# Performance work log

Measured on AMD Instinct MI355X. Metric: run time of the kernel, lower is better.

Reference implementation:

```python
import jax, jax.numpy as jnp
import numpy as np

N_NODES = 50000
N_EDGES = 800000
C_IN = 128
C_OUT = 64
C_HID = 2 * C_OUT  # 128


def setup_inputs() -> dict:
    key = jax.random.key(0)
    ks = jax.random.split(key, 8)
    x = jax.random.normal(ks[0], (N_NODES, C_IN), dtype=jnp.float32)
    edge_index = jax.random.randint(ks[1], (2, N_EDGES), 0, N_NODES, dtype=jnp.int64)
    s1 = 1.0 / np.sqrt(C_IN)
    s2 = 1.0 / np.sqrt(C_HID)
    s3 = 1.0 / np.sqrt(C_OUT)
    W1 = jax.random.uniform(ks[2], (C_IN, C_HID), jnp.float32, -s1, s1)
    b1 = jnp.zeros((C_HID,), jnp.float32)
    W2 = jax.random.uniform(ks[3], (C_HID, C_OUT), jnp.float32, -s2, s2)
    b2 = jnp.zeros((C_OUT,), jnp.float32)
    Wb = jax.random.uniform(ks[4], (1, C_OUT, C_OUT), jnp.float32, -s3, s3)
    bb = jax.random.uniform(ks[5], (1,), jnp.float32, -s3, s3)
    return {"x": x, "edge_index": edge_index, "W1": W1, "b1": b1,
            "W2": W2, "b2": b2, "Wb": Wb, "bb": bb}


def gcn_conv(x, W, b, src, dst, n_nodes):
    # PyG GCNConv: h = x @ W; add self-loops; symmetric normalization D^-1/2 (A+I) D^-1/2.
    h = x @ W  # [N, F]
    ones = jnp.ones((src.shape[0],), h.dtype)
    deg = jax.ops.segment_sum(ones, dst, num_segments=n_nodes) + 1.0  # +1 for self-loop
    dinv = jax.lax.rsqrt(deg)
    norm = dinv[src] * dinv[dst]  # [E]
    msgs = h[src] * norm[:, None]  # [E, F]
    agg = jax.ops.segment_sum(msgs, dst, num_segments=n_nodes)
    # self-loop contribution: norm_ii = 1/deg_i
    agg = agg + h * (1.0 / deg)[:, None]
    return agg + b


def reference(x, edge_index, W1, b1, W2, b2, Wb, bb):
    src = edge_index[0]
    dst = edge_index[1]
    n = x.shape[0]
    # encode
    h = jax.nn.relu(gcn_conv(x, W1, b1, src, dst, n))
    z = gcn_conv(h, W2, b2, src, dst, n)  # [N, C_OUT]
    # decode: bilinear on (z[src], z[dst]) -> sigmoid
    zs = z[src]  # [E, C_OUT]
    zd = z[dst]  # [E, C_OUT]
    logits = jnp.einsum('ec,ocd,ed->eo', zs, Wb, zd) + bb  # [E, 1]
    return jax.nn.sigmoid(logits)
```

## Files before the change

### kernel.cpp

```cpp
#include <hip/hip_runtime.h>
#include <hip/hip_bf16.h>


#define N_NODES 50000
#define BSH 7
#define BSZ 128
#define NBUCK ((N_NODES + BSZ - 1) / BSZ)
#define EPB 4096
#define CAP 3072
#define DSPLIT 4

typedef unsigned int u32;
typedef unsigned short u16;
typedef unsigned long long u64;

typedef __attribute__((ext_vector_type(8))) short bf16x8;
typedef __attribute__((ext_vector_type(4))) float f32x4;
union frag_u { bf16x8 f; u32 u[4]; uint4 v; };

__device__ __forceinline__ float bflo(u32 u) { return __uint_as_float(u << 16); }
__device__ __forceinline__ float bfhi(u32 u) { return __uint_as_float(u & 0xffff0000u); }
__device__ __forceinline__ u32 f2bf(float f) {
    u32 b = __float_as_uint(f);
    return (b + 0x7fffu + ((b >> 16) & 1u)) >> 16;
}
__device__ __forceinline__ u32 pack2(float a, float b) { return f2bf(a) | (f2bf(b) << 16); }

__global__ __launch_bounds__(256) void gemm1_scatter(
        const float* __restrict__ X, const float* __restrict__ W,
        u16* __restrict__ O, int n_rows, int gblk,
        const int* __restrict__ src, const int* __restrict__ dst,
        int* __restrict__ bcur, u64* __restrict__ pair, int E) {
    constexpr int K = 128, NOUT = 128;
    constexpr int KP = K + 8;
    constexpr int NT = NOUT / 16;
    constexpr int KS = K / 32;
    __shared__ __align__(16) char smem[NOUT * KP * 2 * sizeof(u16)];
    int t = threadIdx.x;

    if ((int)blockIdx.x < gblk) {
        u16* Wt_hi = (u16*)smem;
        u16* Wt_lo = Wt_hi + NOUT * KP;
        for (int i4 = t; i4 < K * NOUT / 4; i4 += 256) {
            int k = (i4 * 4) / NOUT;
            int n0 = (i4 * 4) % NOUT;
            float4 w4 = *(const float4*)&W[(size_t)k * NOUT + n0];
            float wv[4] = {w4.x, w4.y, w4.z, w4.w};
#pragma unroll
            for (int q = 0; q < 4; q++) {
                u32 hi = f2bf(wv[q]);
                u32 lo = f2bf(wv[q] - bflo(hi));
                Wt_hi[(n0 + q) * KP + k] = (u16)hi;
                Wt_lo[(n0 + q) * KP + k] = (u16)lo;
            }
        }
        __syncthreads();

        int wave = t >> 6;
        int lane = t & 63;
        int m16 = lane & 15;
        int quad = lane >> 4;
        int row0 = blockIdx.x * 128 + wave * 32;

        f32x4 acc[2][NT] = {};
        for (int ks = 0; ks < KS; ks++) {
            frag_u a_hi[2], a_lo[2];
#pragma unroll
            for (int mt = 0; mt < 2; mt++) {
                int row = row0 + mt * 16 + m16;
                row = row < n_rows ? row : n_rows - 1;
                const float* Xp = X + (size_t)row * K + ks * 32 + quad * 8;
                float4 x0 = *(const float4*)Xp;
                float4 x1 = *(const float4*)(Xp + 4);
                float xv[8] = {x0.x, x0.y, x0.z, x0.w, x1.x, x1.y, x1.z, x1.w};
#pragma unroll
                for (int p = 0; p < 4; p++) {
                    u32 h0 = f2bf(xv[2 * p]), h1 = f2bf(xv[2 * p + 1]);
                    a_hi[mt].u[p] = h0 | (h1 << 16);
                    a_lo[mt].u[p] = pack2(xv[2 * p] - bflo(h0), xv[2 * p + 1] - bflo(h1));
                }
            }
#pragma unroll
            for (int nt = 0; nt < NT; nt++) {
                int n = nt * 16 + m16;
                frag_u b_hi, b_lo;
                b_hi.v = *(const uint4*)&Wt_hi[n * KP + ks * 32 + quad * 8];
                b_lo.v = *(const uint4*)&Wt_lo[n * KP + ks * 32 + quad * 8];
#pragma unroll
                for (int mt = 0; mt < 2; mt++) {
                    acc[mt][nt] = __builtin_amdgcn_mfma_f32_16x16x32_bf16(a_hi[mt].f, b_hi.f, acc[mt][nt], 0, 0, 0);
                    acc[mt][nt] = __builtin_amdgcn_mfma_f32_16x16x32_bf16(a_hi[mt].f, b_lo.f, acc[mt][nt], 0, 0, 0);
                    acc[mt][nt] = __builtin_amdgcn_mfma_f32_16x16x32_bf16(a_lo[mt].f, b_hi.f, acc[mt][nt], 0, 0, 0);
                }
            }
        }
#pragma unroll
        for (int mt = 0; mt < 2; mt++)
#pragma unroll
            for (int nt = 0; nt < NT; nt++)
#pragma unroll
                for (int r = 0; r < 4; r++) {
                    int row = row0 + mt * 16 + quad * 4 + r;
                    if (row < n_rows)
                        O[(size_t)row * NOUT + nt * 16 + m16] = (u16)f2bf(acc[mt][nt][r]);
                }
    } else {
        int* hist = (int*)smem;
        for (int i = t; i < NBUCK; i += 256) hist[i] = 0;
        __syncthreads();
        int base = ((int)blockIdx.x - gblk) * EPB;
        int s_[16], d_[16];
#pragma unroll
        for (int it = 0; it < 16; it++) {
            int e = base + it * 256 + t;
            if (e < E) {
                s_[it] = src[e];
                d_[it] = dst[e];
                atomicAdd(&hist[d_[it] >> BSH], 1);
            } else {
                d_[it] = -1;
            }
        }
        __syncthreads();
        for (int b = t; b < NBUCK; b += 256) {
            int c = hist[b];
            hist[b] = c ? (b * CAP + atomicAdd(&bcur[b], c)) : 0;
        }
        __syncthreads();
#pragma unroll
        for (int it = 0; it < 16; it++) {
            if (d_[it] >= 0) {
                int b = d_[it] >> BSH;
                int off = atomicAdd(&hist[b], 1);
                int e = base + it * 256 + t;
                pair[off] = (u64)((u32)s_[it] | ((u32)(d_[it] & (BSZ - 1)) << 16))
                          | ((u64)(u32)e << 32);
            }
        }
    }
}

__global__ __launch_bounds__(256) void bucket_sort(const u64* __restrict__ pair,
                                                   const int* __restrict__ bcur,
                                                   int* __restrict__ row_ptr,
                                                   int* __restrict__ col,
                                                   float* __restrict__ dinv,
                                                   float* __restrict__ inv, int n, int E) {
    __shared__ int ssum[256];
    __shared__ int cnt[BSZ];
    __shared__ int scn[BSZ];
    __shared__ int cur[BSZ];
    int t = threadIdx.x;
    int base = blockIdx.x << BSH;
    int nn = min(BSZ, n - base);
    int accp = 0;
    for (int i = t; i < (int)blockIdx.x; i += 256) accp += bcur[i];
    ssum[t] = accp;
    __syncthreads();
    for (int s = 128; s > 0; s >>= 1) {
        if (t < s) ssum[t] += ssum[t + s];
        __syncthreads();
    }
    int b0 = ssum[0];
    int cntE = bcur[blockIdx.x];
    int p0 = blockIdx.x * CAP;
    if (t < BSZ) cnt[t] = 0;
    __syncthreads();
    for (int j = t; j < cntE; j += 256)
        atomicAdd(&cnt[(int)((pair[p0 + j] >> 16) & (BSZ - 1))], 1);
    __syncthreads();
    if (t < BSZ) scn[t] = cnt[t];
    __syncthreads();
    for (int off = 1; off < BSZ; off <<= 1) {
        int a = (t < BSZ && t >= off) ? scn[t - off] : 0;
        __syncthreads();
        if (t < BSZ) scn[t] += a;
        __syncthreads();
    }
    if (t < nn) {
        int excl = b0 + scn[t] - cnt[t];
        row_ptr[base + t] = excl;
        cur[t] = excl;
        float d = (float)cnt[t] + 1.0f;
        dinv[base + t] = rsqrtf(d);
        inv[base + t] = 1.0f / d;
    }
    if (t == 0 && blockIdx.x == NBUCK - 1) row_ptr[n] = E;
    __syncthreads();
    for (int j = t; j < cntE; j += 256) {
        u64 p = pair[p0 + j];
        int ln = (int)((p >> 16) & (BSZ - 1));
        int pos = atomicAdd(&cur[ln], 1);
        col[pos] = (int)(p & 0xffffu);
    }
}

template <int K, int NOUT>
__global__ __launch_bounds__(256) void gemm_mfma_bf(const u16* __restrict__ Xv,
                                                    const float* __restrict__ W,
                                                    u16* __restrict__ O, int n_rows) {
    constexpr int KP = K + 8;
    constexpr int NT = NOUT / 16;
    constexpr int KS = K / 32;
    __shared__ __align__(16) u16 Wt_hi[NOUT * KP];
    __shared__ __align__(16) u16 Wt_lo[NOUT * KP];
    int t = threadIdx.x;
    for (int i4 = t; i4 < K * NOUT / 4; i4 += 256) {
        int k = (i4 * 4) / NOUT;
        int n0 = (i4 * 4) % NOUT;
        float4 w4 = *(const float4*)&W[(size_t)k * NOUT + n0];
        float wv[4] = {w4.x, w4.y, w4.z, w4.w};
#pragma unroll
        for (int q = 0; q < 4; q++) {
            u32 hi = f2bf(wv[q]);
            u32 lo = f2bf(wv[q] - bflo(hi));
            Wt_hi[(n0 + q) * KP + k] = (u16)hi;
            Wt_lo[(n0 + q) * KP + k] = (u16)lo;
        }
    }
    __syncthreads();

    int wave = t >> 6;
    int lane = t & 63;
    int m16 = lane & 15;
    int quad = lane >> 4;
    int row0 = blockIdx.x * 128 + wave * 32;

    f32x4 acc[2][NT] = {};
    for (int ks = 0; ks < KS; ks++) {
        frag_u a_hi[2];
#pragma unroll
        for (int mt = 0; mt < 2; mt++) {
            int row = row0 + mt * 16 + m16;
            row = row < n_rows ? row : n_rows - 1;
            a_hi[mt].v = *(const uint4*)(Xv + (size_t)row * K + ks * 32 + quad * 8);
        }
#pragma unroll
        for (int nt = 0; nt < NT; nt++) {
            int n = nt * 16 + m16;
            frag_u b_hi, b_lo;
            b_hi.v = *(const uint4*)&Wt_hi[n * KP + ks * 32 + quad * 8];
            b_lo.v = *(const uint4*)&Wt_lo[n * KP + ks * 32 + quad * 8];
#pragma unroll
            for (int mt = 0; mt < 2; mt++) {
                acc[mt][nt] = __builtin_amdgcn_mfma_f32_16x16x32_bf16(a_hi[mt].f, b_hi.f, acc[mt][nt], 0, 0, 0);
                acc[mt][nt] = __builtin_amdgcn_mfma_f32_16x16x32_bf16(a_hi[mt].f, b_lo.f, acc[mt][nt], 0, 0, 0);
            }
        }
    }
#pragma unroll
    for (int mt = 0; mt < 2; mt++)
#pragma unroll
        for (int nt = 0; nt < NT; nt++)
#pragma unroll
            for (int r = 0; r < 4; r++) {
                int row = row0 + mt * 16 + quad * 4 + r;
                if (row < n_rows)
                    O[(size_t)row * NOUT + nt * 16 + m16] = (u16)f2bf(acc[mt][nt][r]);
            }
}

template <int C, bool RELU>
__global__ __launch_bounds__(256) void agg_pull(const u16* __restrict__ H,
                                                const int* __restrict__ row_ptr,
                                                const int* __restrict__ col,
                                                const float* __restrict__ dinv,
                                                const float* __restrict__ inv,
                                                const float* __restrict__ b,
                                                u16* __restrict__ O, int n) {
    constexpr int TPN = C / 8;
    const uint4* Hv = (const uint4*)H;
    int tid = blockIdx.x * 256 + threadIdx.x;
    int node = tid / TPN;
    if (node >= n) return;
    int part = tid % TPN;
    int c8 = part * 8;
    float dn = dinv[node];
    float iv = inv[node];
    float acc[8];
    {
        uint4 h = Hv[(size_t)node * TPN + part];
        acc[0] = bflo(h.x) * iv + b[c8 + 0];
        acc[1] = bfhi(h.x) * iv + b[c8 + 1];
        acc[2] = bflo(h.y) * iv + b[c8 + 2];
        acc[3] = bfhi(h.y) * iv + b[c8 + 3];
        acc[4] = bflo(h.z) * iv + b[c8 + 4];
        acc[5] = bfhi(h.z) * iv + b[c8 + 5];
        acc[6] = bflo(h.w) * iv + b[c8 + 6];
        acc[7] = bfhi(h.w) * iv + b[c8 + 7];
    }
    int j = row_ptr[node];
    int end = row_ptr[node + 1];
    for (; j + 3 < end; j += 4) {
        int s0 = col[j], s1 = col[j + 1], s2 = col[j + 2], s3 = col[j + 3];
        float n0 = dn * dinv[s0], n1 = dn * dinv[s1];
        float n2 = dn * dinv[s2], n3 = dn * dinv[s3];
        uint4 v0 = Hv[(size_t)s0 * TPN + part];
        uint4 v1 = Hv[(size_t)s1 * TPN + part];
        uint4 v2 = Hv[(size_t)s2 * TPN + part];
        uint4 v3 = Hv[(size_t)s3 * TPN + part];
        acc[0] += bflo(v0.x) * n0 + bflo(v1.x) * n1 + bflo(v2.x) * n2 + bflo(v3.x) * n3;
        acc[1] += bfhi(v0.x) * n0 + bfhi(v1.x) * n1 + bfhi(v2.x) * n2 + bfhi(v3.x) * n3;
        acc[2] += bflo(v0.y) * n0 + bflo(v1.y) * n1 + bflo(v2.y) * n2 + bflo(v3.y) * n3;
        acc[3] += bfhi(v0.y) * n0 + bfhi(v1.y) * n1 + bfhi(v2.y) * n2 + bfhi(v3.y) * n3;
        acc[4] += bflo(v0.z) * n0 + bflo(v1.z) * n1 + bflo(v2.z) * n2 + bflo(v3.z) * n3;
        acc[5] += bfhi(v0.z) * n0 + bfhi(v1.z) * n1 + bfhi(v2.z) * n2 + bfhi(v3.z) * n3;
        acc[6] += bflo(v0.w) * n0 + bflo(v1.w) * n1 + bflo(v2.w) * n2 + bflo(v3.w) * n3;
        acc[7] += bfhi(v0.w) * n0 + bfhi(v1.w) * n1 + bfhi(v2.w) * n2 + bfhi(v3.w) * n3;
    }
    for (; j < end; j++) {
        int s = col[j];
        float nm = dn * dinv[s];
        uint4 v = Hv[(size_t)s * TPN + part];
        acc[0] += bflo(v.x) * nm; acc[1] += bfhi(v.x) * nm;
        acc[2] += bflo(v.y) * nm; acc[3] += bfhi(v.y) * nm;
        acc[4] += bflo(v.z) * nm; acc[5] += bfhi(v.z) * nm;
        acc[6] += bflo(v.w) * nm; acc[7] += bfhi(v.w) * nm;
    }
    if (RELU) {
#pragma unroll
        for (int i = 0; i < 8; i++) acc[i] = fmaxf(acc[i], 0.f);
    }
    uint4 o;
    o.x = pack2(acc[0], acc[1]);
    o.y = pack2(acc[2], acc[3]);
    o.z = pack2(acc[4], acc[5]);
    o.w = pack2(acc[6], acc[7]);
    ((uint4*)O)[(size_t)node * TPN + part] = o;
}

__global__ __launch_bounds__(256) void decode_fused(const u16* __restrict__ Z,
                                                    const float* __restrict__ Wb,
                                                    const u64* __restrict__ pair,
                                                    const int* __restrict__ bcur,
                                                    const float* __restrict__ bb,
                                                    float* __restrict__ out, int n) {
    constexpr int K = 64, NOUT = 64;
    constexpr int KP = K + 8;
    constexpr int QP = 72;
    __shared__ __align__(16) u16 Wt_hi[NOUT * KP];
    __shared__ __align__(16) u16 Wt_lo[NOUT * KP];
    __shared__ __align__(16) u16 Qs[BSZ * QP];
    int t = threadIdx.x;
    int bucket = blockIdx.x / DSPLIT;
    int part = blockIdx.x % DSPLIT;
    int base = bucket << BSH;

    for (int i4 = t; i4 < K * NOUT / 4; i4 += 256) {
        int nn_ = (i4 * 4) / K;
        int k0 = (i4 * 4) % K;
        float4 w4 = *(const float4*)&Wb[(size_t)nn_ * K + k0];
        float wv[4] = {w4.x, w4.y, w4.z, w4.w};
#pragma unroll
        for (int q = 0; q < 4; q++) {
            u32 hi = f2bf(wv[q]);
            u32 lo = f2bf(wv[q] - bflo(hi));
            Wt_hi[nn_ * KP + k0 + q] = (u16)hi;
            Wt_lo[nn_ * KP + k0 + q] = (u16)lo;
        }
    }
    __syncthreads();

    {
        int wave = t >> 6;
        int lane = t & 63;
        int m16 = lane & 15;
        int quad = lane >> 4;
        int row0 = wave * 32;
        f32x4 acc[2][4] = {};
        for (int ks = 0; ks < 2; ks++) {
            frag_u a[2];
#pragma unroll
            for (int mt = 0; mt < 2; mt++) {
                int node = base + row0 + mt * 16 + m16;
                node = node < n ? node : n - 1;
                a[mt].v = *(const uint4*)(Z + (size_t)node * K + ks * 32 + quad * 8);
            }
#pragma unroll
            for (int nt = 0; nt < 4; nt++) {
                int nc = nt * 16 + m16;
                frag_u b_hi, b_lo;
                b_hi.v = *(const uint4*)&Wt_hi[nc * KP + ks * 32 + quad * 8];
                b_lo.v = *(const uint4*)&Wt_lo[nc * KP + ks * 32 + quad * 8];
#pragma unroll
                for (int mt = 0; mt < 2; mt++) {
                    acc[mt][nt] = __builtin_amdgcn_mfma_f32_16x16x32_bf16(a[mt].f, b_hi.f, acc[mt][nt], 0, 0, 0);
                    acc[mt][nt] = __builtin_amdgcn_mfma_f32_16x16x32_bf16(a[mt].f, b_lo.f, acc[mt][nt], 0, 0, 0);
                }
            }
        }
#pragma unroll
        for (int mt = 0; mt < 2; mt++)
#pragma unroll
            for (int nt = 0; nt < 4; nt++)
#pragma unroll
                for (int r = 0; r < 4; r++) {
                    int rl = row0 + mt * 16 + quad * 4 + r;
                    Qs[rl * QP + nt * 16 + m16] = (u16)f2bf(acc[mt][nt][r]);
                }
    }
    __syncthreads();

    const uint4* Zv = (const uint4*)Z;
    int cntE = bcur[bucket];
    int p0 = bucket * CAP;
    int chunk = (cntE + DSPLIT - 1) / DSPLIT;
    int s0 = part * chunk;
    int s1 = min(s0 + chunk, cntE);
    float bbv = bb[0];
    int lane8 = t & 7;
    for (int j = s0 + (t >> 3); j < s1; j += 32) {
        u64 p = pair[p0 + j];
        int s = (int)(p & 0xffffu);
        int loc = (int)((p >> 16) & (BSZ - 1));
        int eid = (int)(p >> 32);
        uint4 z = Zv[(size_t)s * 8 + lane8];
        uint4 q = *(const uint4*)&Qs[loc * QP + lane8 * 8];
        float pd = bflo(z.x) * bflo(q.x) + bfhi(z.x) * bfhi(q.x)
                 + bflo(z.y) * bflo(q.y) + bfhi(z.y) * bfhi(q.y)
                 + bflo(z.z) * bflo(q.z) + bfhi(z.z) * bfhi(q.z)
                 + bflo(z.w) * bflo(q.w) + bfhi(z.w) * bfhi(q.w);
        pd += __shfl_down(pd, 4, 8);
        pd += __shfl_down(pd, 2, 8);
        pd += __shfl_down(pd, 1, 8);
        if (lane8 == 0) out[eid] = 1.0f / (1.0f + expf(-(pd + bbv)));
    }
}

extern "C" void kernel_launch(void* const* d_in, const int* in_sizes, int n_in,
                              void* d_out, int out_size, void* d_ws, size_t ws_size,
                              hipStream_t stream) {
    const float* x  = (const float*)d_in[0];
    const int*   ei = (const int*)d_in[1];
    const float* W1 = (const float*)d_in[2];
    const float* b1 = (const float*)d_in[3];
    const float* W2 = (const float*)d_in[4];
    const float* b2 = (const float*)d_in[5];
    const float* Wb = (const float*)d_in[6];
    const float* bb = (const float*)d_in[7];
    float* out = (float*)d_out;

    const int N = N_NODES;
    const int E = in_sizes[1] / 2;
    const int* src = ei;
    const int* dst = ei + E;
    const int GBLK = (N + 127) / 128;
    const int SBLK = (E + EPB - 1) / EPB;

    char* w = (char*)d_ws;
    int*   bcur    = (int*)w;   w += (size_t)512 * 4;
    int*   row_ptr = (int*)w;   w += (size_t)(N + 1) * 4;
    int*   col     = (int*)w;   w += (size_t)E * 4;
    w = (char*)(((size_t)w + 15) & ~(size_t)15);
    u64*   pair    = (u64*)w;   w += (size_t)NBUCK * CAP * 8;
    float* dinv    = (float*)w; w += (size_t)N * 4;
    float* inv     = (float*)w; w += (size_t)N * 4;
    w = (char*)(((size_t)w + 15) & ~(size_t)15);
    u16* bufA = (u16*)w;        w += (size_t)N * 128 * 2;
    u16* bufB = (u16*)w;        w += (size_t)N * 128 * 2;
    u16* bufC = (u16*)w;

    u16* H1 = bufA;
    u16* h1 = bufB;
    u16* H2 = bufA;
    u16* Z  = bufC;

    hipMemsetAsync(bcur, 0, 512 * 4, stream);
    gemm1_scatter<<<GBLK + SBLK, 256, 0, stream>>>(x, W1, H1, N, GBLK,
                                                   src, dst, bcur, pair, E);
    bucket_sort<<<NBUCK, 256, 0, stream>>>(pair, bcur, row_ptr, col, dinv, inv, N, E);

    agg_pull<128, true><<<((size_t)N * 16 + 255) / 256, 256, 0, stream>>>(
        H1, row_ptr, col, dinv, inv, b1, h1, N);

    gemm_mfma_bf<128, 64><<<GBLK, 256, 0, stream>>>(h1, W2, H2, N);
    agg_pull<64, false><<<((size_t)N * 8 + 255) / 256, 256, 0, stream>>>(
        H2, row_ptr, col, dinv, inv, b2, Z, N);

    decode_fused<<<NBUCK * DSPLIT, 256, 0, stream>>>(Z, Wb, pair, bcur, bb, out, N);
}
```

Baseline: 232.4 us.

## Store node features in 32-channel planes to shrink gather working set

Changes the H1/h1/H2/Z feature buffers from row-major [N,C] to planar [C/32][N][32] layout, updating the GEMM writers/readers, the aggregation kernel and the decode gather. The aggregation now processes one 32-channel plane at a time across all nodes, so the random neighbor gathers in a pass touch a smaller (N*64 byte) region that fits better in cache. The trade-off is that each neighbor gather is 64B per plane instead of a full row, so col/dinv are re-read once per plane, and the GEMM stores become more strided.

After: 257.6 us. +10.8%, slower.

```diff
diff --git a/kernel.cpp b/kernel.cpp
--- a/kernel.cpp
+++ b/kernel.cpp
@@ -101,8 +101,9 @@
 #pragma unroll
                 for (int r = 0; r < 4; r++) {
                     int row = row0 + mt * 16 + quad * 4 + r;
+                    int c = nt * 16 + m16;
                     if (row < n_rows)
-                        O[(size_t)row * NOUT + nt * 16 + m16] = (u16)f2bf(acc[mt][nt][r]);
+                        O[((size_t)(c >> 5) * n_rows + row) * 32 + (c & 31)] = (u16)f2bf(acc[mt][nt][r]);
                 }
     } else {
         int* hist = (int*)smem;
@@ -233,7 +234,7 @@
         for (int mt = 0; mt < 2; mt++) {
             int row = row0 + mt * 16 + m16;
             row = row < n_rows ? row : n_rows - 1;
-            a_hi[mt].v = *(const uint4*)(Xv + (size_t)row * K + ks * 32 + quad * 8);
+            a_hi[mt].v = *(const uint4*)(Xv + ((size_t)ks * n_rows + row) * 32 + quad * 8);
         }
 #pragma unroll
         for (int nt = 0; nt < NT; nt++) {
@@ -255,31 +256,35 @@
 #pragma unroll
             for (int r = 0; r < 4; r++) {
                 int row = row0 + mt * 16 + quad * 4 + r;
+                int c = nt * 16 + m16;
                 if (row < n_rows)
-                    O[(size_t)row * NOUT + nt * 16 + m16] = (u16)f2bf(acc[mt][nt][r]);
+                    O[((size_t)(c >> 5) * n_rows + row) * 32 + (c & 31)] = (u16)f2bf(acc[mt][nt][r]);
             }
 }
 
 template <int C, bool RELU>
-__global__ __launch_bounds__(256) void agg_pull(const u16* __restrict__ H,
-                                                const int* __restrict__ row_ptr,
-                                                const int* __restrict__ col,
-                                                const float* __restrict__ dinv,
-                                                const float* __restrict__ inv,
-                                                const float* __restrict__ b,
-                                                u16* __restrict__ O, int n) {
-    constexpr int TPN = C / 8;
+__global__ __launch_bounds__(256) void agg_pull_plane(const u16* __restrict__ H,
+                                                      const int* __restrict__ row_ptr,
+                                                      const int* __restrict__ col,
+                                                      const float* __restrict__ dinv,
+                                                      const float* __restrict__ inv,
+                                                      const float* __restrict__ b,
+                                                      u16* __restrict__ O, int n) {
+    constexpr int PL = C / 32;
     const uint4* Hv = (const uint4*)H;
-    int tid = blockIdx.x * 256 + threadIdx.x;
-    int node = tid / TPN;
-    if (node >= n) return;
-    int part = tid % TPN;
-    int c8 = part * 8;
+    int item = blockIdx.x * 256 + threadIdx.x;
+    if (item >= PL * n * 4) return;
+    int plane = item / (n * 4);
+    int rem = item - plane * (n * 4);
+    int node = rem >> 2;
+    int part = rem & 3;
+    int c8 = plane * 32 + part * 8;
+    size_t pb = (size_t)plane * n * 4;
     float dn = dinv[node];
     float iv = inv[node];
     float acc[8];
     {
-        uint4 h = Hv[(size_t)node * TPN + part];
+        uint4 h = Hv[pb + (size_t)node * 4 + part];
         acc[0] = bflo(h.x) * iv + b[c8 + 0];
         acc[1] = bfhi(h.x) * iv + b[c8 + 1];
         acc[2] = bflo(h.y) * iv + b[c8 + 2];
@@ -295,10 +300,10 @@
         int s0 = col[j], s1 = col[j + 1], s2 = col[j + 2], s3 = col[j + 3];
         float n0 = dn * dinv[s0], n1 = dn * dinv[s1];
         float n2 = dn * dinv[s2], n3 = dn * dinv[s3];
-        uint4 v0 = Hv[(size_t)s0 * TPN + part];
-        uint4 v1 = Hv[(size_t)s1 * TPN + part];
-        uint4 v2 = Hv[(size_t)s2 * TPN + part];
-        uint4 v3 = Hv[(size_t)s3 * TPN + part];
+        uint4 v0 = Hv[pb + (size_t)s0 * 4 + part];
+        uint4 v1 = Hv[pb + (size_t)s1 * 4 + part];
+        uint4 v2 = Hv[pb + (size_t)s2 * 4 + part];
+        uint4 v3 = Hv[pb + (size_t)s3 * 4 + part];
         acc[0] += bflo(v0.x) * n0 + bflo(v1.x) * n1 + bflo(v2.x) * n2 + bflo(v3.x) * n3;
         acc[1] += bfhi(v0.x) * n0 + bfhi(v1.x) * n1 + bfhi(v2.x) * n2 + bfhi(v3.x) * n3;
         acc[2] += bflo(v0.y) * n0 + bflo(v1.y) * n1 + bflo(v2.y) * n2 + bflo(v3.y) * n3;
@@ -311,7 +316,7 @@
     for (; j < end; j++) {
         int s = col[j];
         float nm = dn * dinv[s];
-        uint4 v = Hv[(size_t)s * TPN + part];
+        uint4 v = Hv[pb + (size_t)s * 4 + part];
         acc[0] += bflo(v.x) * nm; acc[1] += bfhi(v.x) * nm;
         acc[2] += bflo(v.y) * nm; acc[3] += bfhi(v.y) * nm;
         acc[4] += bflo(v.z) * nm; acc[5] += bfhi(v.z) * nm;
@@ -326,7 +331,7 @@
     o.y = pack2(acc[2], acc[3]);
     o.z = pack2(acc[4], acc[5]);
     o.w = pack2(acc[6], acc[7]);
-    ((uint4*)O)[(size_t)node * TPN + part] = o;
+    ((uint4*)O)[pb + (size_t)node * 4 + part] = o;
 }
 
 __global__ __launch_bounds__(256) void decode_fused(const u16* __restrict__ Z,
@@ -374,7 +379,7 @@
             for (int mt = 0; mt < 2; mt++) {
                 int node = base + row0 + mt * 16 + m16;
                 node = node < n ? node : n - 1;
-                a[mt].v = *(const uint4*)(Z + (size_t)node * K + ks * 32 + quad * 8);
+                a[mt].v = *(const uint4*)(Z + ((size_t)ks * n + node) * 32 + quad * 8);
             }
 #pragma unroll
             for (int nt = 0; nt < 4; nt++) {
@@ -409,12 +414,13 @@
     int s1 = min(s0 + chunk, cntE);
     float bbv = bb[0];
     int lane8 = t & 7;
+    size_t zb = (size_t)(lane8 >> 2) * n * 4;
     for (int j = s0 + (t >> 3); j < s1; j += 32) {
         u64 p = pair[p0 + j];
         int s = (int)(p & 0xffffu);
         int loc = (int)((p >> 16) & (BSZ - 1));
         int eid = (int)(p >> 32);
-        uint4 z = Zv[(size_t)s * 8 + lane8];
+        uint4 z = Zv[zb + (size_t)s * 4 + (lane8 & 3)];
         uint4 q = *(const uint4*)&Qs[loc * QP + lane8 * 8];
         float pd = bflo(z.x) * bflo(q.x) + bfhi(z.x) * bfhi(q.x)
                  + bflo(z.y) * bflo(q.y) + bfhi(z.y) * bfhi(q.y)
@@ -470,11 +476,11 @@
                                                    src, dst, bcur, pair, E);
     bucket_sort<<<NBUCK, 256, 0, stream>>>(pair, bcur, row_ptr, col, dinv, inv, N, E);
 
-    agg_pull<128, true><<<((size_t)N * 16 + 255) / 256, 256, 0, stream>>>(
+    agg_pull_plane<128, true><<<((size_t)N * 16 + 255) / 256, 256, 0, stream>>>(
         H1, row_ptr, col, dinv, inv, b1, h1, N);
 
     gemm_mfma_bf<128, 64><<<GBLK, 256, 0, stream>>>(h1, W2, H2, N);
-    agg_pull<64, false><<<((size_t)N * 8 + 255) / 256, 256, 0, stream>>>(
+    agg_pull_plane<64, false><<<((size_t)N * 8 + 255) / 256, 256, 0, stream>>>(
         H2, row_ptr, col, dinv, inv, b2, Z, N);
 
     decode_fused<<<NBUCK * DSPLIT, 256, 0, stream>>>(Z, Wb, pair, bcur, bb, out, N);
```
